# Kernel tuning notes

Measured on AMD Instinct MI355X. Metric: run time of the kernel, lower is better.

The kernel has to match this reference:

```python
import jax, jax.numpy as jnp
import numpy as np
import math

B, S, E, H = 8, 1024, 512, 8
EPS = 1e-5

def _ln(x, g, b):
    mu = jnp.mean(x, axis=-1, keepdims=True)
    var = jnp.mean(jnp.square(x - mu), axis=-1, keepdims=True)
    return (x - mu) * jax.lax.rsqrt(var + EPS) * g + b

def setup_inputs() -> dict:
    key = jax.random.key(0)
    ks = iter(jax.random.split(key, 40))
    def w(shape, scale=0.02):
        return jax.random.normal(next(ks), shape, dtype=jnp.float32) * scale
    inp = {
        'x': jax.random.normal(next(ks), (B, S, E), dtype=jnp.float32),
        'cond': jax.random.normal(next(ks), (B, 1, E), dtype=jnp.float32),
        # AdaLN modulation linears (stored as (in,out))
        'g1w': w((E, E)), 'g1b': jnp.zeros((E,), jnp.float32),
        'be1w': w((E, E)), 'be1b': jnp.zeros((E,), jnp.float32),
        'a1w': w((E, E)), 'a1b': jnp.zeros((E,), jnp.float32),
        'g2w': w((E, E)), 'g2b': jnp.zeros((E,), jnp.float32),
        'be2w': w((E, E)), 'be2b': jnp.zeros((E,), jnp.float32),
        'a2w': w((E, E)), 'a2b': jnp.zeros((E,), jnp.float32),
        # LayerNorm affine
        'ln1g': jnp.ones((E,), jnp.float32), 'ln1b': jnp.zeros((E,), jnp.float32),
        'ln2g': jnp.ones((E,), jnp.float32), 'ln2b': jnp.zeros((E,), jnp.float32),
        # attention projections: each head has width E -> out dim H*E
        'wq': w((E, H * E)), 'bq': jnp.zeros((H * E,), jnp.float32),
        'wk': w((E, H * E)), 'bk': jnp.zeros((H * E,), jnp.float32),
        'wv': w((E, H * E)), 'bv': jnp.zeros((H * E,), jnp.float32),
        'lvw': w((H * E, E)), 'lvb': jnp.zeros((E,), jnp.float32),
        # FFN
        'f1w': w((E, 4 * E)), 'f1b': jnp.zeros((4 * E,), jnp.float32),
        'f2w': w((4 * E, E)), 'f2b': jnp.zeros((E,), jnp.float32),
    }
    return inp

def reference(x, cond, g1w, g1b, be1w, be1b, a1w, a1b, g2w, g2b, be2w, be2b, a2w, a2b,
              ln1g, ln1b, ln2g, ln2b, wq, bq, wk, bk, wv, bv, lvw, lvb, f1w, f1b, f2w, f2b):
    # AdaLN modulation signals, each (B,1,E)
    gamma1 = cond @ g1w + g1b
    beta1 = cond @ be1w + be1b
    alpha1 = cond @ a1w + a1b
    gamma2 = cond @ g2w + g2b
    beta2 = cond @ be2w + be2b
    alpha2 = cond @ a2w + a2b

    y = _ln(x, ln1g, ln1b) * (1.0 + gamma1) + beta1
    q = (y @ wq + bq).reshape(B, S, H, E).transpose(0, 2, 1, 3)  # (B,H,S,E)
    k = (y @ wk + bk).reshape(B, S, H, E).transpose(0, 2, 1, 3)
    v = (y @ wv + bv).reshape(B, S, H, E).transpose(0, 2, 1, 3)
    # NOTE: original scales by sqrt(q.size(2)) == sqrt(seq_len), not head_dim
    scale = 1.0 / math.sqrt(S)
    attn = jax.nn.softmax(jnp.einsum('bhse,bhte->bhst', q, k) * scale, axis=-1)
    o = jnp.einsum('bhst,bhte->bhse', attn, v)  # (B,H,S,E)
    o = o.transpose(0, 2, 1, 3).reshape(B, S, H * E)
    y = x + (o @ lvw + lvb) * alpha1

    z = _ln(y, ln2g, ln2b) * (1.0 + gamma2) + beta2
    z = (jax.nn.relu(z @ f1w + f1b) @ f2w + f2b) * alpha2
    return y + z
```

## Files before the change

kernel.cpp:

```cpp
#include <hip/hip_runtime.h>
#include <hip/hip_bf16.h>

typedef __bf16 bf16_t;
typedef bf16_t bf16x8 __attribute__((ext_vector_type(8)));
typedef bf16_t bf16x4 __attribute__((ext_vector_type(4)));
typedef float f32x4 __attribute__((ext_vector_type(4)));

#define LDSK 40

typedef const __attribute__((address_space(1))) void GV;
typedef __attribute__((address_space(3))) void LV;

__device__ __forceinline__ void gload_lds16(const bf16_t* gsrc, bf16_t* ldst) {
    __builtin_amdgcn_global_load_lds((GV*)gsrc, (LV*)ldst, 16, 0, 0);
}

__global__ __launch_bounds__(256) void wtrans_kernel(const float* __restrict__ in,
                                                     bf16_t* __restrict__ out, int K, int N)
{
    __shared__ float tile[32][33];
    const int n0 = blockIdx.x * 32, k0 = blockIdx.y * 32;
    const int tx = threadIdx.x & 31, ty = threadIdx.x >> 5;
#pragma unroll
    for (int i = 0; i < 32; i += 8)
        tile[ty + i][tx] = in[(long long)(k0 + ty + i) * N + n0 + tx];
    __syncthreads();
#pragma unroll
    for (int i = 0; i < 32; i += 8)
        out[(long long)(n0 + ty + i) * K + k0 + tx] = (bf16_t)tile[tx][ty + i];
}

__global__ __launch_bounds__(256) void modsig_kernel(
    const float* __restrict__ cond,
    const float* __restrict__ w0, const float* __restrict__ w1, const float* __restrict__ w2,
    const float* __restrict__ w3, const float* __restrict__ w4, const float* __restrict__ w5,
    const float* __restrict__ c0, const float* __restrict__ c1, const float* __restrict__ c2,
    const float* __restrict__ c3, const float* __restrict__ c4, const float* __restrict__ c5,
    float* __restrict__ out)
{
    __shared__ float cs[512];
    const int sig = blockIdx.x >> 3, b = blockIdx.x & 7;
    const float* w; const float* bi;
    switch (sig) {
        case 0: w = w0; bi = c0; break;
        case 1: w = w1; bi = c1; break;
        case 2: w = w2; bi = c2; break;
        case 3: w = w3; bi = c3; break;
        case 4: w = w4; bi = c4; break;
        default: w = w5; bi = c5; break;
    }
    for (int i = threadIdx.x; i < 512; i += 256) cs[i] = cond[b * 512 + i];
    __syncthreads();
    for (int n = threadIdx.x; n < 512; n += 256) {
        float s = bi[n];
        for (int i = 0; i < 512; ++i) s = fmaf(cs[i], w[(long long)i * 512 + n], s);
        out[(long long)(sig * 8 + b) * 512 + n] = s;
    }
}

__global__ __launch_bounds__(128) void ln_mod_kernel(
    const float* __restrict__ x, const float* __restrict__ g, const float* __restrict__ be,
    const float* __restrict__ gamma, const float* __restrict__ beta, bf16_t* __restrict__ out)
{
    const int row = blockIdx.x;
    const int b = row >> 10;
    const int t = threadIdx.x;
    const float4 v = reinterpret_cast<const float4*>(x + (long long)row * 512)[t];
    float s = v.x + v.y + v.z + v.w;
    float ss = v.x * v.x + v.y * v.y + v.z * v.z + v.w * v.w;
    for (int o = 32; o; o >>= 1) { s += __shfl_xor(s, o); ss += __shfl_xor(ss, o); }
    __shared__ float red[4];
    if ((t & 63) == 0) { red[t >> 6] = s; red[2 + (t >> 6)] = ss; }
    __syncthreads();
    s = red[0] + red[1]; ss = red[2] + red[3];
    const float mu = s * (1.f / 512.f);
    const float rstd = rsqrtf(ss * (1.f / 512.f) - mu * mu + 1e-5f);
    const float4 gv = reinterpret_cast<const float4*>(g)[t];
    const float4 bv = reinterpret_cast<const float4*>(be)[t];
    const float4 ga = reinterpret_cast<const float4*>(gamma + b * 512)[t];
    const float4 bb = reinterpret_cast<const float4*>(beta + b * 512)[t];
    bf16x4 ov;
    ov[0] = (bf16_t)(((v.x - mu) * rstd * gv.x + bv.x) * (1.f + ga.x) + bb.x);
    ov[1] = (bf16_t)(((v.y - mu) * rstd * gv.y + bv.y) * (1.f + ga.y) + bb.y);
    ov[2] = (bf16_t)(((v.z - mu) * rstd * gv.z + bv.z) * (1.f + ga.z) + bb.z);
    ov[3] = (bf16_t)(((v.w - mu) * rstd * gv.w + bv.w) * (1.f + ga.w) + bb.w);
    reinterpret_cast<bf16x4*>(out + (long long)row * 512)[t] = ov;
}

template <int EPI>
__global__ __launch_bounds__(256) void gemm128_kernel(
    const bf16_t* __restrict__ A, const bf16_t* __restrict__ B,
    const float* __restrict__ bias, void* Cout,
    int M, int N, int K, int lda, int ldb, int ldc)
{
    const int m0 = blockIdx.y * 128, n0 = blockIdx.x * 128;
    const int tid = threadIdx.x, lane = tid & 63, wid = tid >> 6;
    const int wr = wid >> 1, wc = wid & 1;

    __shared__ bf16_t As[128][LDSK];
    __shared__ bf16_t Bs[128][LDSK];

    f32x4 acc[4][4];
#pragma unroll
    for (int m = 0; m < 4; ++m)
#pragma unroll
        for (int n = 0; n < 4; ++n) acc[m][n] = (f32x4){0.f, 0.f, 0.f, 0.f};

    const int srow = tid >> 2;
    const int skoff = (tid & 3) * 8;
    const long long aRow0 = (long long)(m0 + srow) * lda + skoff;
    const long long aRow1 = (long long)(m0 + srow + 64) * lda + skoff;
    const long long bRow0 = (long long)(n0 + srow) * ldb + skoff;
    const long long bRow1 = (long long)(n0 + srow + 64) * ldb + skoff;
    const int frow = lane & 15;
    const int fko = (lane >> 4) << 3;

    for (int kt = 0; kt < K; kt += 32) {
        const uint4 a0 = *reinterpret_cast<const uint4*>(A + aRow0 + kt);
        const uint4 a1 = *reinterpret_cast<const uint4*>(A + aRow1 + kt);
        const uint4 b0 = *reinterpret_cast<const uint4*>(B + bRow0 + kt);
        const uint4 b1 = *reinterpret_cast<const uint4*>(B + bRow1 + kt);
        *reinterpret_cast<uint4*>(&As[srow][skoff]) = a0;
        *reinterpret_cast<uint4*>(&As[srow + 64][skoff]) = a1;
        *reinterpret_cast<uint4*>(&Bs[srow][skoff]) = b0;
        *reinterpret_cast<uint4*>(&Bs[srow + 64][skoff]) = b1;
        __syncthreads();
        bf16x8 af[4], bfv[4];
#pragma unroll
        for (int m = 0; m < 4; ++m)
            af[m] = *reinterpret_cast<const bf16x8*>(&As[wr * 64 + m * 16 + frow][fko]);
#pragma unroll
        for (int n = 0; n < 4; ++n)
            bfv[n] = *reinterpret_cast<const bf16x8*>(&Bs[wc * 64 + n * 16 + frow][fko]);
#pragma unroll
        for (int m = 0; m < 4; ++m)
#pragma unroll
            for (int n = 0; n < 4; ++n)
                acc[m][n] = __builtin_amdgcn_mfma_f32_16x16x32_bf16(af[m], bfv[n], acc[m][n], 0, 0, 0);
        __syncthreads();
    }

#pragma unroll
    for (int m = 0; m < 4; ++m) {
        const int gm = m0 + wr * 64 + m * 16 + ((lane >> 4) << 2);
#pragma unroll
        for (int n = 0; n < 4; ++n) {
            const int gn = n0 + wc * 64 + n * 16 + (lane & 15);
            const float bb = bias ? bias[gn] : 0.f;
#pragma unroll
            for (int j = 0; j < 4; ++j) {
                const float v = acc[m][n][j] + bb;
                const int gmj = gm + j;
                if (EPI == 0) {
                    ((bf16_t*)Cout)[(long long)gmj * ldc + gn] = (bf16_t)v;
                } else if (EPI == 1) {
                    ((bf16_t*)Cout)[(long long)gmj * ldc + gn] = (bf16_t)fmaxf(v, 0.f);
                } else {
                    const long long ci =
                        (long long)(((gmj >> 10) * 8 + (gn >> 9)) * 512 + (gn & 511)) * 1024 + (gmj & 1023);
                    ((bf16_t*)Cout)[ci] = (bf16_t)v;
                }
            }
        }
    }
}

__global__ __launch_bounds__(256) void gemm64_kernel(
    const bf16_t* __restrict__ A, const bf16_t* __restrict__ B,
    const float* __restrict__ bias, float* __restrict__ Cout,
    const float* __restrict__ resid, const float* __restrict__ alpha,
    int M, int N, int K, int lda, int ldb)
{
    const int m0 = blockIdx.y * 64, n0 = blockIdx.x * 128;
    const int tid = threadIdx.x, lane = tid & 63, wid = tid >> 6;
    const int wr = wid >> 1, wc = wid & 1;

    __shared__ bf16_t As[64][LDSK];
    __shared__ bf16_t Bs[128][LDSK];

    f32x4 acc[2][4];
#pragma unroll
    for (int m = 0; m < 2; ++m)
#pragma unroll
        for (int n = 0; n < 4; ++n) acc[m][n] = (f32x4){0.f, 0.f, 0.f, 0.f};

    const int srow = tid >> 2;
    const int skoff = (tid & 3) * 8;
    const long long aRow = (long long)(m0 + srow) * lda + skoff;
    const long long bRow0 = (long long)(n0 + srow) * ldb + skoff;
    const long long bRow1 = (long long)(n0 + srow + 64) * ldb + skoff;
    const int frow = lane & 15;
    const int fko = (lane >> 4) << 3;

    for (int kt = 0; kt < K; kt += 32) {
        const uint4 a0 = *reinterpret_cast<const uint4*>(A + aRow + kt);
        const uint4 b0 = *reinterpret_cast<const uint4*>(B + bRow0 + kt);
        const uint4 b1 = *reinterpret_cast<const uint4*>(B + bRow1 + kt);
        *reinterpret_cast<uint4*>(&As[srow][skoff]) = a0;
        *reinterpret_cast<uint4*>(&Bs[srow][skoff]) = b0;
        *reinterpret_cast<uint4*>(&Bs[srow + 64][skoff]) = b1;
        __syncthreads();
        bf16x8 af[2], bfv[4];
#pragma unroll
        for (int m = 0; m < 2; ++m)
            af[m] = *reinterpret_cast<const bf16x8*>(&As[wr * 32 + m * 16 + frow][fko]);
#pragma unroll
        for (int n = 0; n < 4; ++n)
            bfv[n] = *reinterpret_cast<const bf16x8*>(&Bs[wc * 64 + n * 16 + frow][fko]);
#pragma unroll
        for (int m = 0; m < 2; ++m)
#pragma unroll
            for (int n = 0; n < 4; ++n)
                acc[m][n] = __builtin_amdgcn_mfma_f32_16x16x32_bf16(af[m], bfv[n], acc[m][n], 0, 0, 0);
        __syncthreads();
    }

#pragma unroll
    for (int m = 0; m < 2; ++m) {
        const int gm = m0 + wr * 32 + m * 16 + ((lane >> 4) << 2);
#pragma unroll
        for (int n = 0; n < 4; ++n) {
            const int gn = n0 + wc * 64 + n * 16 + (lane & 15);
            const float bb = bias[gn];
#pragma unroll
            for (int j = 0; j < 4; ++j) {
                const int gmj = gm + j;
                const long long ci = (long long)gmj * 512 + gn;
                Cout[ci] = resid[ci] + (acc[m][n][j] + bb) * alpha[(gmj >> 10) * 512 + gn];
            }
        }
    }
}

#define FA_LDS 140288
__global__ __launch_bounds__(512, 2) void flash_kernel(
    bf16_t* __restrict__ qb, const bf16_t* __restrict__ kb, const bf16_t* __restrict__ vtb)
{
    extern __shared__ char smem[];
    bf16_t* Qs = (bf16_t*)smem;
    bf16_t* KVs = (bf16_t*)(smem + 65536);
    char* PB = smem + 131072;
    float* pmax = (float*)(smem + 139264);
    float* psum = (float*)(smem + 139776);

    const int bid = blockIdx.x;
    const int xcd = bid & 7, idx = bid >> 3;
    const int qt = idx & 15, bhl = idx >> 4;
    const int bh = xcd * 8 + bhl;
    const int b = bh >> 3, h = bh & 7;
    const int q0 = qt * 64;
    const int tid = threadIdx.x, lane = tid & 63, wid = tid >> 6;
    const int laneq = lane & 15, lx = lane & 7, lg = lane >> 4;
    const int wk = wid >> 2, wq = wid & 3;
    const int we = wid & 3, wq2 = wid >> 2;

#pragma unroll
    for (int r = 0; r < 8; ++r) {
        const int row = r * 8 + wid;
        const bf16_t* src = qb + ((long long)(b * 1024 + q0 + row) * 8 + h) * 512
                            + ((lane ^ (row & 7)) << 3);
        gload_lds16(src, Qs + row * 512);
    }

    f32x4 accA[8], accB[8];
#pragma unroll
    for (int e = 0; e < 8; ++e) { accA[e] = (f32x4){0.f,0.f,0.f,0.f}; accB[e] = (f32x4){0.f,0.f,0.f,0.f}; }
    float mS = -1e30f, mPA = -1e30f, mPB = -1e30f, lA = 0.f, lB = 0.f;

    const int rA0 = wk * 32 + laneq, rA1 = rA0 + 16;
    const int rQ = wq * 16 + laneq;
    const int qi = wq * 16 + laneq;
    const int qA = wq2 * 32 + laneq, qB = qA + 16;

    for (int t = 0; t < 16; ++t) {
        const int kv0 = t * 64;
#pragma unroll
        for (int r = 0; r < 8; ++r) {
            const int row = r * 8 + wid;
            const bf16_t* src = kb + ((long long)(b * 1024 + kv0 + row) * 8 + h) * 512
                                + ((lane ^ (row & 7)) << 3);
            gload_lds16(src, KVs + row * 512);
        }
        __syncthreads();

        f32x4 s0 = (f32x4){0.f,0.f,0.f,0.f}, s1 = (f32x4){0.f,0.f,0.f,0.f};
        const char* KsB = (const char*)KVs;
        const char* QsB = (const char*)Qs;
#pragma unroll 4
        for (int ks = 0; ks < 16; ++ks) {
            const int cb = ks * 4 + lg;
            const int co = (cb ^ lx) << 4;
            bf16x8 a0 = *(const bf16x8*)(KsB + rA0 * 1024 + co);
            bf16x8 a1 = *(const bf16x8*)(KsB + rA1 * 1024 + co);
            bf16x8 bq = *(const bf16x8*)(QsB + rQ * 1024 + co);
            s0 = __builtin_amdgcn_mfma_f32_16x16x32_bf16(a0, bq, s0, 0, 0, 0);
            s1 = __builtin_amdgcn_mfma_f32_16x16x32_bf16(a1, bq, s1, 0, 0, 0);
        }
        float sc[8];
#pragma unroll
        for (int j = 0; j < 4; ++j) { sc[j] = s0[j] * 0.03125f; sc[4 + j] = s1[j] * 0.03125f; }
        float mloc = sc[0];
#pragma unroll
        for (int j = 1; j < 8; ++j) mloc = fmaxf(mloc, sc[j]);
        mloc = fmaxf(mloc, __shfl_xor(mloc, 16));
        mloc = fmaxf(mloc, __shfl_xor(mloc, 32));
        if (lane < 16) pmax[wk * 64 + wq * 16 + lane] = mloc;
        __syncthreads();

        const float mnew = fmaxf(mS, fmaxf(pmax[qi], pmax[64 + qi]));
        mS = mnew;
        float pe[8]; float sl = 0.f;
#pragma unroll
        for (int j = 0; j < 8; ++j) { pe[j] = __expf(sc[j] - mnew); sl += pe[j]; }
        sl += __shfl_xor(sl, 16);
        sl += __shfl_xor(sl, 32);
        if (lane < 16) psum[wk * 64 + wq * 16 + lane] = sl;
        {
            bf16x4 p0, p1;
#pragma unroll
            for (int j = 0; j < 4; ++j) { p0[j] = (bf16_t)pe[j]; p1[j] = (bf16_t)pe[4 + j]; }
            const int kc0 = wk * 8 + lg, kc1 = kc0 + 4;
            const int qx = (qi & 7) << 1;
            *(bf16x4*)(PB + qi * 128 + ((kc0 ^ qx) << 3)) = p0;
            *(bf16x4*)(PB + qi * 128 + ((kc1 ^ qx) << 3)) = p1;
        }
#pragma unroll
        for (int r = 0; r < 8; ++r) {
            const int e = r * 64 + wid * 8 + (lane >> 3);
            const bf16_t* src = vtb + ((long long)bh * 512 + e) * 1024 + kv0
                                + (((lane & 7) ^ (e & 7)) << 3);
            gload_lds16(src, KVs + (r * 64 + wid * 8) * 64);
        }
        __syncthreads();

        {
            const float mnA = fmaxf(mPA, fmaxf(pmax[qA], pmax[64 + qA]));
            const float rA = __expf(mPA - mnA);
            mPA = mnA;
            lA = lA * rA + psum[qA] + psum[64 + qA];
            const float mnB = fmaxf(mPB, fmaxf(pmax[qB], pmax[64 + qB]));
            const float rB = __expf(mPB - mnB);
            mPB = mnB;
            lB = lB * rB + psum[qB] + psum[64 + qB];
#pragma unroll
            for (int e = 0; e < 8; ++e) {
#pragma unroll
                for (int j = 0; j < 4; ++j) { accA[e][j] *= rA; accB[e][j] *= rB; }
            }
        }
        const char* VB = (const char*)KVs;
        const int qxA = (qA & 7) << 1, qxB = (qB & 7) << 1;
#pragma unroll
        for (int ks2 = 0; ks2 < 2; ++ks2) {
            const int kcp = ks2 * 8 + lg * 2;
            bf16x8 pA = *(const bf16x8*)(PB + qA * 128 + ((kcp ^ qxA) << 3));
            bf16x8 pBv = *(const bf16x8*)(PB + qB * 128 + ((kcp ^ qxB) << 3));
            const int kcv = ks2 * 4 + lg;
#pragma unroll
            for (int ef = 0; ef < 8; ++ef) {
                const int re = we * 128 + ef * 16 + laneq;
                bf16x8 av = *(const bf16x8*)(VB + re * 128 + ((kcv ^ lx) << 4));
                accA[ef] = __builtin_amdgcn_mfma_f32_16x16x32_bf16(av, pA, accA[ef], 0, 0, 0);
                accB[ef] = __builtin_amdgcn_mfma_f32_16x16x32_bf16(av, pBv, accB[ef], 0, 0, 0);
            }
        }
        __syncthreads();
    }

    const float iA = 1.f / lA, iB = 1.f / lB;
#pragma unroll
    for (int ef = 0; ef < 8; ++ef) {
        const int e0 = we * 128 + ef * 16 + lg * 4;
        bf16x4 oA, oB;
#pragma unroll
        for (int j = 0; j < 4; ++j) { oA[j] = (bf16_t)(accA[ef][j] * iA); oB[j] = (bf16_t)(accB[ef][j] * iB); }
        *(bf16x4*)(qb + ((long long)(b * 1024 + q0 + qA) * 8 + h) * 512 + e0) = oA;
        *(bf16x4*)(qb + ((long long)(b * 1024 + q0 + qB) * 8 + h) * 512 + e0) = oB;
    }
}

extern "C" void kernel_launch(void* const* d_in, const int* in_sizes, int n_in,
                              void* d_out, int out_size, void* d_ws, size_t ws_size,
                              hipStream_t stream)
{
    const float* x    = (const float*)d_in[0];
    const float* cond = (const float*)d_in[1];
    const float* g1w  = (const float*)d_in[2];  const float* g1b  = (const float*)d_in[3];
    const float* be1w = (const float*)d_in[4];  const float* be1b = (const float*)d_in[5];
    const float* a1w  = (const float*)d_in[6];  const float* a1b  = (const float*)d_in[7];
    const float* g2w  = (const float*)d_in[8];  const float* g2b  = (const float*)d_in[9];
    const float* be2w = (const float*)d_in[10]; const float* be2b = (const float*)d_in[11];
    const float* a2w  = (const float*)d_in[12]; const float* a2b  = (const float*)d_in[13];
    const float* ln1g = (const float*)d_in[14]; const float* ln1b = (const float*)d_in[15];
    const float* ln2g = (const float*)d_in[16]; const float* ln2b = (const float*)d_in[17];
    const float* wq   = (const float*)d_in[18]; const float* bq   = (const float*)d_in[19];
    const float* wk   = (const float*)d_in[20]; const float* bk   = (const float*)d_in[21];
    const float* wv   = (const float*)d_in[22]; const float* bv   = (const float*)d_in[23];
    const float* lvw  = (const float*)d_in[24]; const float* lvb  = (const float*)d_in[25];
    const float* f1w  = (const float*)d_in[26]; const float* f1b  = (const float*)d_in[27];
    const float* f2w  = (const float*)d_in[28]; const float* f2b  = (const float*)d_in[29];
    (void)in_sizes; (void)n_in; (void)out_size; (void)ws_size;

    char* w8 = (char*)d_ws;
    float*  mod  = (float*)(w8);
    bf16_t* wqT  = (bf16_t*)(w8 + 98304);
    bf16_t* wkT  = (bf16_t*)(w8 + 98304 + 4194304);
    bf16_t* wvT  = (bf16_t*)(w8 + 98304 + 2 * 4194304);
    bf16_t* lvwT = (bf16_t*)(w8 + 98304 + 3 * 4194304);
    bf16_t* f1wT = (bf16_t*)(w8 + 98304 + 4 * 4194304);
    bf16_t* f2wT = (bf16_t*)(w8 + 98304 + 4 * 4194304 + 2097152);
    bf16_t* ybf  = (bf16_t*)(w8 + 98304 + 4 * 4194304 + 2 * 2097152);
    bf16_t* qb   = (bf16_t*)(w8 + 98304 + 4 * 4194304 + 2 * 2097152 + 8388608);
    bf16_t* kb   = qb + 33554432;
    bf16_t* vtb  = kb + 33554432;

    static int fa_attr_done = 0;
    if (!fa_attr_done) {
        (void)hipFuncSetAttribute((const void*)flash_kernel,
                                  hipFuncAttributeMaxDynamicSharedMemorySize, FA_LDS);
        fa_attr_done = 1;
    }

    const dim3 blk(256);
    wtrans_kernel<<<dim3(128, 16), blk, 0, stream>>>(wq, wqT, 512, 4096);
    wtrans_kernel<<<dim3(128, 16), blk, 0, stream>>>(wk, wkT, 512, 4096);
    wtrans_kernel<<<dim3(128, 16), blk, 0, stream>>>(wv, wvT, 512, 4096);
    wtrans_kernel<<<dim3(16, 128), blk, 0, stream>>>(lvw, lvwT, 4096, 512);
    wtrans_kernel<<<dim3(64, 16), blk, 0, stream>>>(f1w, f1wT, 512, 2048);
    wtrans_kernel<<<dim3(16, 64), blk, 0, stream>>>(f2w, f2wT, 2048, 512);
    modsig_kernel<<<48, blk, 0, stream>>>(cond, g1w, be1w, a1w, g2w, be2w, a2w,
                                          g1b, be1b, a1b, g2b, be2b, a2b, mod);
    ln_mod_kernel<<<8192, 128, 0, stream>>>(x, ln1g, ln1b, mod, mod + 4096, ybf);
    gemm128_kernel<0><<<dim3(32, 64), blk, 0, stream>>>(ybf, wqT, bq, qb,
        8192, 4096, 512, 512, 512, 4096);
    gemm128_kernel<0><<<dim3(32, 64), blk, 0, stream>>>(ybf, wkT, bk, kb,
        8192, 4096, 512, 512, 512, 4096);
    gemm128_kernel<3><<<dim3(32, 64), blk, 0, stream>>>(ybf, wvT, bv, vtb,
        8192, 4096, 512, 512, 512, 0);
    flash_kernel<<<1024, 512, FA_LDS, stream>>>(qb, kb, vtb);
    gemm64_kernel<<<dim3(4, 128), blk, 0, stream>>>(qb, lvwT, lvb, (float*)d_out, x, mod + 8192,
        8192, 512, 4096, 4096, 4096);
    ln_mod_kernel<<<8192, 128, 0, stream>>>((const float*)d_out, ln2g, ln2b,
                                            mod + 12288, mod + 16384, ybf);
    gemm128_kernel<1><<<dim3(16, 64), blk, 0, stream>>>(ybf, f1wT, f1b, qb,
        8192, 2048, 512, 512, 512, 2048);
    gemm64_kernel<<<dim3(4, 128), blk, 0, stream>>>(qb, f2wT, f2b, (float*)d_out,
        (const float*)d_out, mod + 20480,
        8192, 512, 2048, 2048, 2048);
}
```

Baseline: 729.1 us.

## Restructure flash attention pipeline and use direct-to-LDS swizzled GEMM loads

The GEMM kernels now stage tiles with global_load_lds into XOR-swizzled unpadded LDS and raise wave priority around the MFMA loops. The flash kernel keeps Q fragments in registers and splits the buffer into separate K and V regions, so the next K tile and the V tile are prefetched while compute runs. It also double-buffers the row max/sum exchange to drop one barrier per tile and switches to exp2 with a log2-folded scale. Accumulator rescaling is deferred and skipped when no max changed, which aims to cut exp and multiply work and synchronization at the cost of more registers and subtler numerics.

```diff
diff --git a/kernel.cpp b/kernel.cpp
--- a/kernel.cpp
+++ b/kernel.cpp
@@ -5,8 +5,6 @@
 typedef bf16_t bf16x8 __attribute__((ext_vector_type(8)));
 typedef bf16_t bf16x4 __attribute__((ext_vector_type(4)));
 typedef float f32x4 __attribute__((ext_vector_type(4)));
-
-#define LDSK 40
 
 typedef const __attribute__((address_space(1))) void GV;
 typedef __attribute__((address_space(3))) void LV;
@@ -97,8 +95,8 @@
     const int tid = threadIdx.x, lane = tid & 63, wid = tid >> 6;
     const int wr = wid >> 1, wc = wid & 1;
 
-    __shared__ bf16_t As[128][LDSK];
-    __shared__ bf16_t Bs[128][LDSK];
+    __shared__ bf16_t As[4096];
+    __shared__ bf16_t Bs[4096];
 
     f32x4 acc[4][4];
 #pragma unroll
@@ -106,37 +104,40 @@
 #pragma unroll
         for (int n = 0; n < 4; ++n) acc[m][n] = (f32x4){0.f, 0.f, 0.f, 0.f};
 
-    const int srow = tid >> 2;
-    const int skoff = (tid & 3) * 8;
-    const long long aRow0 = (long long)(m0 + srow) * lda + skoff;
-    const long long aRow1 = (long long)(m0 + srow + 64) * lda + skoff;
-    const long long bRow0 = (long long)(n0 + srow) * ldb + skoff;
-    const long long bRow1 = (long long)(n0 + srow + 64) * ldb + skoff;
-    const int frow = lane & 15;
-    const int fko = (lane >> 4) << 3;
+    const int r0 = wid * 16 + (lane >> 2);
+    const int lc = (lane & 3) ^ ((lane >> 2) & 3);
+    const long long aOff0 = (long long)(m0 + r0) * lda + lc * 8;
+    const long long aOff1 = (long long)(m0 + r0 + 64) * lda + lc * 8;
+    const long long bOff0 = (long long)(n0 + r0) * ldb + lc * 8;
+    const long long bOff1 = (long long)(n0 + r0 + 64) * ldb + lc * 8;
+    bf16_t* aDst0 = As + wid * 512;
+    bf16_t* aDst1 = As + 2048 + wid * 512;
+    bf16_t* bDst0 = Bs + wid * 512;
+    bf16_t* bDst1 = Bs + 2048 + wid * 512;
+
+    const int frow = lane & 15, lg = lane >> 4;
+    const int pc = lg ^ (frow & 3);
 
     for (int kt = 0; kt < K; kt += 32) {
-        const uint4 a0 = *reinterpret_cast<const uint4*>(A + aRow0 + kt);
-        const uint4 a1 = *reinterpret_cast<const uint4*>(A + aRow1 + kt);
-        const uint4 b0 = *reinterpret_cast<const uint4*>(B + bRow0 + kt);
-        const uint4 b1 = *reinterpret_cast<const uint4*>(B + bRow1 + kt);
-        *reinterpret_cast<uint4*>(&As[srow][skoff]) = a0;
-        *reinterpret_cast<uint4*>(&As[srow + 64][skoff]) = a1;
-        *reinterpret_cast<uint4*>(&Bs[srow][skoff]) = b0;
-        *reinterpret_cast<uint4*>(&Bs[srow + 64][skoff]) = b1;
+        gload_lds16(A + aOff0 + kt, aDst0);
+        gload_lds16(A + aOff1 + kt, aDst1);
+        gload_lds16(B + bOff0 + kt, bDst0);
+        gload_lds16(B + bOff1 + kt, bDst1);
         __syncthreads();
         bf16x8 af[4], bfv[4];
 #pragma unroll
         for (int m = 0; m < 4; ++m)
-            af[m] = *reinterpret_cast<const bf16x8*>(&As[wr * 64 + m * 16 + frow][fko]);
+            af[m] = *reinterpret_cast<const bf16x8*>(As + (wr * 64 + m * 16 + frow) * 32 + pc * 8);
 #pragma unroll
         for (int n = 0; n < 4; ++n)
-            bfv[n] = *reinterpret_cast<const bf16x8*>(&Bs[wc * 64 + n * 16 + frow][fko]);
+            bfv[n] = *reinterpret_cast<const bf16x8*>(Bs + (wc * 64 + n * 16 + frow) * 32 + pc * 8);
+        __builtin_amdgcn_s_setprio(1);
 #pragma unroll
         for (int m = 0; m < 4; ++m)
 #pragma unroll
             for (int n = 0; n < 4; ++n)
                 acc[m][n] = __builtin_amdgcn_mfma_f32_16x16x32_bf16(af[m], bfv[n], acc[m][n], 0, 0, 0);
+        __builtin_amdgcn_s_setprio(0);
         __syncthreads();
     }
 
@@ -175,8 +176,8 @@
     const int tid = threadIdx.x, lane = tid & 63, wid = tid >> 6;
     const int wr = wid >> 1, wc = wid & 1;
 
-    __shared__ bf16_t As[64][LDSK];
-    __shared__ bf16_t Bs[128][LDSK];
+    __shared__ bf16_t As[2048];
+    __shared__ bf16_t Bs[4096];
 
     f32x4 acc[2][4];
 #pragma unroll
@@ -184,34 +185,37 @@
 #pragma unroll
         for (int n = 0; n < 4; ++n) acc[m][n] = (f32x4){0.f, 0.f, 0.f, 0.f};
 
-    const int srow = tid >> 2;
-    const int skoff = (tid & 3) * 8;
-    const long long aRow = (long long)(m0 + srow) * lda + skoff;
-    const long long bRow0 = (long long)(n0 + srow) * ldb + skoff;
-    const long long bRow1 = (long long)(n0 + srow + 64) * ldb + skoff;
-    const int frow = lane & 15;
-    const int fko = (lane >> 4) << 3;
+    const int r0 = wid * 16 + (lane >> 2);
+    const int lc = (lane & 3) ^ ((lane >> 2) & 3);
+    const long long aOff0 = (long long)(m0 + r0) * lda + lc * 8;
+    const long long bOff0 = (long long)(n0 + r0) * ldb + lc * 8;
+    const long long bOff1 = (long long)(n0 + r0 + 64) * ldb + lc * 8;
+    bf16_t* aDst0 = As + wid * 512;
+    bf16_t* bDst0 = Bs + wid * 512;
+    bf16_t* bDst1 = Bs + 2048 + wid * 512;
+
+    const int frow = lane & 15, lg = lane >> 4;
+    const int pc = lg ^ (frow & 3);
 
     for (int kt = 0; kt < K; kt += 32) {
-        const uint4 a0 = *reinterpret_cast<const uint4*>(A + aRow + kt);
-        const uint4 b0 = *reinterpret_cast<const uint4*>(B + bRow0 + kt);
-        const uint4 b1 = *reinterpret_cast<const uint4*>(B + bRow1 + kt);
-        *reinterpret_cast<uint4*>(&As[srow][skoff]) = a0;
-        *reinterpret_cast<uint4*>(&Bs[srow][skoff]) = b0;
-        *reinterpret_cast<uint4*>(&Bs[srow + 64][skoff]) = b1;
+        gload_lds16(A + aOff0 + kt, aDst0);
+        gload_lds16(B + bOff0 + kt, bDst0);
+        gload_lds16(B + bOff1 + kt, bDst1);
         __syncthreads();
         bf16x8 af[2], bfv[4];
 #pragma unroll
         for (int m = 0; m < 2; ++m)
-            af[m] = *reinterpret_cast<const bf16x8*>(&As[wr * 32 + m * 16 + frow][fko]);
+            af[m] = *reinterpret_cast<const bf16x8*>(As + (wr * 32 + m * 16 + frow) * 32 + pc * 8);
 #pragma unroll
         for (int n = 0; n < 4; ++n)
-            bfv[n] = *reinterpret_cast<const bf16x8*>(&Bs[wc * 64 + n * 16 + frow][fko]);
+            bfv[n] = *reinterpret_cast<const bf16x8*>(Bs + (wc * 64 + n * 16 + frow) * 32 + pc * 8);
+        __builtin_amdgcn_s_setprio(1);
 #pragma unroll
         for (int m = 0; m < 2; ++m)
 #pragma unroll
             for (int n = 0; n < 4; ++n)
                 acc[m][n] = __builtin_amdgcn_mfma_f32_16x16x32_bf16(af[m], bfv[n], acc[m][n], 0, 0, 0);
+        __builtin_amdgcn_s_setprio(0);
         __syncthreads();
     }
 
@@ -232,16 +236,17 @@
     }
 }
 
-#define FA_LDS 140288
+#define FA_LDS 141312
+#define SCL 0.04508422132207354f
 __global__ __launch_bounds__(512, 2) void flash_kernel(
     bf16_t* __restrict__ qb, const bf16_t* __restrict__ kb, const bf16_t* __restrict__ vtb)
 {
     extern __shared__ char smem[];
-    bf16_t* Qs = (bf16_t*)smem;
-    bf16_t* KVs = (bf16_t*)(smem + 65536);
+    bf16_t* Ks = (bf16_t*)smem;
+    bf16_t* Vs = (bf16_t*)(smem + 65536);
     char* PB = smem + 131072;
-    float* pmax = (float*)(smem + 139264);
-    float* psum = (float*)(smem + 139776);
+    float* pmaxB = (float*)(smem + 139264);
+    float* psumB = (float*)(smem + 140288);
 
     const int bid = blockIdx.x;
     const int xcd = bid & 7, idx = bid >> 3;
@@ -257,99 +262,84 @@
 #pragma unroll
     for (int r = 0; r < 8; ++r) {
         const int row = r * 8 + wid;
-        const bf16_t* src = qb + ((long long)(b * 1024 + q0 + row) * 8 + h) * 512
-                            + ((lane ^ (row & 7)) << 3);
-        gload_lds16(src, Qs + row * 512);
-    }
-
+        gload_lds16(kb + ((long long)(b * 1024 + row) * 8 + h) * 512 + ((lane ^ (row & 7)) << 3),
+                    Ks + row * 512);
+    }
+    const int qi = wq * 16 + laneq;
+    bf16x8 qfrag[16];
+    {
+        const bf16_t* qrow = qb + ((long long)(b * 1024 + q0 + qi) * 8 + h) * 512 + lg * 8;
+#pragma unroll
+        for (int ks = 0; ks < 16; ++ks) qfrag[ks] = *reinterpret_cast<const bf16x8*>(qrow + ks * 32);
+    }
     f32x4 accA[8], accB[8];
 #pragma unroll
     for (int e = 0; e < 8; ++e) { accA[e] = (f32x4){0.f,0.f,0.f,0.f}; accB[e] = (f32x4){0.f,0.f,0.f,0.f}; }
-    float mS = -1e30f, mPA = -1e30f, mPB = -1e30f, lA = 0.f, lB = 0.f;
-
+    float mS = 0.f, mPA = 0.f, mPB = 0.f, lA = 0.f, lB = 0.f;
     const int rA0 = wk * 32 + laneq, rA1 = rA0 + 16;
-    const int rQ = wq * 16 + laneq;
-    const int qi = wq * 16 + laneq;
     const int qA = wq2 * 32 + laneq, qB = qA + 16;
+    const int qx = (qi & 7) << 1;
+    const int qxA = (qA & 7) << 1, qxB = (qB & 7) << 1;
+    __syncthreads();
 
     for (int t = 0; t < 16; ++t) {
         const int kv0 = t * 64;
 #pragma unroll
         for (int r = 0; r < 8; ++r) {
-            const int row = r * 8 + wid;
-            const bf16_t* src = kb + ((long long)(b * 1024 + kv0 + row) * 8 + h) * 512
-                                + ((lane ^ (row & 7)) << 3);
-            gload_lds16(src, KVs + row * 512);
-        }
-        __syncthreads();
-
+            const int e = r * 64 + wid * 8 + (lane >> 3);
+            gload_lds16(vtb + ((long long)bh * 512 + e) * 1024 + kv0 + ((lx ^ (e & 7)) << 3),
+                        Vs + (r * 64 + wid * 8) * 64);
+        }
         f32x4 s0 = (f32x4){0.f,0.f,0.f,0.f}, s1 = (f32x4){0.f,0.f,0.f,0.f};
-        const char* KsB = (const char*)KVs;
-        const char* QsB = (const char*)Qs;
-#pragma unroll 4
+        const char* KsB = (const char*)Ks;
+        __builtin_amdgcn_s_setprio(1);
+#pragma unroll
         for (int ks = 0; ks < 16; ++ks) {
-            const int cb = ks * 4 + lg;
-            const int co = (cb ^ lx) << 4;
+            const int co = ((ks * 4 + lg) ^ lx) << 4;
             bf16x8 a0 = *(const bf16x8*)(KsB + rA0 * 1024 + co);
             bf16x8 a1 = *(const bf16x8*)(KsB + rA1 * 1024 + co);
-            bf16x8 bq = *(const bf16x8*)(QsB + rQ * 1024 + co);
-            s0 = __builtin_amdgcn_mfma_f32_16x16x32_bf16(a0, bq, s0, 0, 0, 0);
-            s1 = __builtin_amdgcn_mfma_f32_16x16x32_bf16(a1, bq, s1, 0, 0, 0);
-        }
-        float sc[8];
-#pragma unroll
-        for (int j = 0; j < 4; ++j) { sc[j] = s0[j] * 0.03125f; sc[4 + j] = s1[j] * 0.03125f; }
-        float mloc = sc[0];
-#pragma unroll
-        for (int j = 1; j < 8; ++j) mloc = fmaxf(mloc, sc[j]);
+            s0 = __builtin_amdgcn_mfma_f32_16x16x32_bf16(a0, qfrag[ks], s0, 0, 0, 0);
+            s1 = __builtin_amdgcn_mfma_f32_16x16x32_bf16(a1, qfrag[ks], s1, 0, 0, 0);
+        }
+        __builtin_amdgcn_s_setprio(0);
+        float f[8];
+#pragma unroll
+        for (int j = 0; j < 4; ++j) { f[j] = s0[j] * SCL; f[4 + j] = s1[j] * SCL; }
+        float mloc = f[0];
+#pragma unroll
+        for (int j = 1; j < 8; ++j) mloc = fmaxf(mloc, f[j]);
         mloc = fmaxf(mloc, __shfl_xor(mloc, 16));
         mloc = fmaxf(mloc, __shfl_xor(mloc, 32));
-        if (lane < 16) pmax[wk * 64 + wq * 16 + lane] = mloc;
-        __syncthreads();
-
-        const float mnew = fmaxf(mS, fmaxf(pmax[qi], pmax[64 + qi]));
-        mS = mnew;
         float pe[8]; float sl = 0.f;
 #pragma unroll
-        for (int j = 0; j < 8; ++j) { pe[j] = __expf(sc[j] - mnew); sl += pe[j]; }
+        for (int j = 0; j < 8; ++j) { pe[j] = exp2f(f[j] - mS); sl += pe[j]; }
         sl += __shfl_xor(sl, 16);
         sl += __shfl_xor(sl, 32);
-        if (lane < 16) psum[wk * 64 + wq * 16 + lane] = sl;
+        if (lane < 16) {
+            pmaxB[(t & 1) * 128 + wk * 64 + wq * 16 + lane] = mloc;
+            psumB[(t & 1) * 128 + wk * 64 + wq * 16 + lane] = sl;
+        }
         {
             bf16x4 p0, p1;
 #pragma unroll
             for (int j = 0; j < 4; ++j) { p0[j] = (bf16_t)pe[j]; p1[j] = (bf16_t)pe[4 + j]; }
             const int kc0 = wk * 8 + lg, kc1 = kc0 + 4;
-            const int qx = (qi & 7) << 1;
             *(bf16x4*)(PB + qi * 128 + ((kc0 ^ qx) << 3)) = p0;
             *(bf16x4*)(PB + qi * 128 + ((kc1 ^ qx) << 3)) = p1;
         }
-#pragma unroll
-        for (int r = 0; r < 8; ++r) {
-            const int e = r * 64 + wid * 8 + (lane >> 3);
-            const bf16_t* src = vtb + ((long long)bh * 512 + e) * 1024 + kv0
-                                + (((lane & 7) ^ (e & 7)) << 3);
-            gload_lds16(src, KVs + (r * 64 + wid * 8) * 64);
-        }
-        __syncthreads();
-
-        {
-            const float mnA = fmaxf(mPA, fmaxf(pmax[qA], pmax[64 + qA]));
-            const float rA = __expf(mPA - mnA);
-            mPA = mnA;
-            lA = lA * rA + psum[qA] + psum[64 + qA];
-            const float mnB = fmaxf(mPB, fmaxf(pmax[qB], pmax[64 + qB]));
-            const float rB = __expf(mPB - mnB);
-            mPB = mnB;
-            lB = lB * rB + psum[qB] + psum[64 + qB];
-#pragma unroll
-            for (int e = 0; e < 8; ++e) {
-#pragma unroll
-                for (int j = 0; j < 4; ++j) { accA[e][j] *= rA; accB[e][j] *= rB; }
+        __syncthreads();
+
+        if (t < 15) {
+#pragma unroll
+            for (int r = 0; r < 8; ++r) {
+                const int row = r * 8 + wid;
+                gload_lds16(kb + ((long long)(b * 1024 + kv0 + 64 + row) * 8 + h) * 512
+                                + ((lane ^ (row & 7)) << 3),
+                            Ks + row * 512);
             }
         }
-        const char* VB = (const char*)KVs;
-        const int qxA = (qA & 7) << 1, qxB = (qB & 7) << 1;
+        const char* VB = (const char*)Vs;
+        __builtin_amdgcn_s_setprio(1);
 #pragma unroll
         for (int ks2 = 0; ks2 < 2; ++ks2) {
             const int kcp = ks2 * 8 + lg * 2;
@@ -363,6 +353,26 @@
                 accA[ef] = __builtin_amdgcn_mfma_f32_16x16x32_bf16(av, pA, accA[ef], 0, 0, 0);
                 accB[ef] = __builtin_amdgcn_mfma_f32_16x16x32_bf16(av, pBv, accB[ef], 0, 0, 0);
             }
+        }
+        __builtin_amdgcn_s_setprio(0);
+        {
+            const float* pmax_t = pmaxB + (t & 1) * 128;
+            const float* psum_t = psumB + (t & 1) * 128;
+            mS = fmaxf(mS, fmaxf(pmax_t[qi], pmax_t[64 + qi]));
+            lA += psum_t[qA] + psum_t[64 + qA];
+            lB += psum_t[qB] + psum_t[64 + qB];
+            const float mnA = fmaxf(mPA, fmaxf(pmax_t[qA], pmax_t[64 + qA]));
+            const float mnB = fmaxf(mPB, fmaxf(pmax_t[qB], pmax_t[64 + qB]));
+            if (__ballot((mnA > mPA) || (mnB > mPB))) {
+                const float rA = exp2f(mPA - mnA), rB = exp2f(mPB - mnB);
+                lA *= rA; lB *= rB;
+#pragma unroll
+                for (int e = 0; e < 8; ++e) {
+#pragma unroll
+                    for (int j = 0; j < 4; ++j) { accA[e][j] *= rA; accB[e][j] *= rB; }
+                }
+            }
+            mPA = mnA; mPB = mnB;
         }
         __syncthreads();
     }
@@ -414,12 +424,8 @@
     bf16_t* kb   = qb + 33554432;
     bf16_t* vtb  = kb + 33554432;
 
-    static int fa_attr_done = 0;
-    if (!fa_attr_done) {
-        (void)hipFuncSetAttribute((const void*)flash_kernel,
-                                  hipFuncAttributeMaxDynamicSharedMemorySize, FA_LDS);
-        fa_attr_done = 1;
-    }
+    (void)hipFuncSetAttribute((const void*)flash_kernel,
+                              hipFuncAttributeMaxDynamicSharedMemorySize, FA_LDS);
 
     const dim3 blk(256);
     wtrans_kernel<<<dim3(128, 16), blk, 0, stream>>>(wq, wqT, 512, 4096);
```

Measured after the change: 713.0 us. -2.2%, faster.
